# Kernel optimization log

Hardware: AMD Instinct MI355X
Metric: run time of the kernel (lower is better)

Reference implementation:

```python
import jax, jax.numpy as jnp
import numpy as np
import math

D_MODEL = 2048
NUM_HEADS = 32
NUM_KV_HEADS = 8
HEAD_DIM = D_MODEL // NUM_HEADS  # 64
BATCH = 2
SEQ = 2048


def setup_inputs() -> dict:
    key = jax.random.key(0)
    ks = jax.random.split(key, 5)
    std_q = math.sqrt(2.0 / (D_MODEL + D_MODEL))
    std_kv = math.sqrt(2.0 / (D_MODEL + NUM_KV_HEADS * HEAD_DIM))
    x = jax.random.normal(ks[0], (BATCH, SEQ, D_MODEL), dtype=jnp.float32)
    Wq = jax.random.normal(ks[1], (D_MODEL, D_MODEL), dtype=jnp.float32) * std_q
    Wk = jax.random.normal(ks[2], (NUM_KV_HEADS * HEAD_DIM, D_MODEL), dtype=jnp.float32) * std_kv
    Wv = jax.random.normal(ks[3], (NUM_KV_HEADS * HEAD_DIM, D_MODEL), dtype=jnp.float32) * std_kv
    Wo = jax.random.normal(ks[4], (D_MODEL, D_MODEL), dtype=jnp.float32) * std_q
    return {"x": x, "Wq": Wq, "Wk": Wk, "Wv": Wv, "Wo": Wo}


def reference(x, Wq, Wk, Wv, Wo):
    B, L, _ = x.shape
    group = NUM_HEADS // NUM_KV_HEADS
    # projections: x @ W.T
    q = (x @ Wq.T).reshape(B, L, NUM_HEADS, HEAD_DIM).transpose(0, 2, 1, 3)      # [B,H,L,D]
    k = (x @ Wk.T).reshape(B, L, NUM_KV_HEADS, HEAD_DIM).transpose(0, 2, 1, 3)   # [B,Hkv,L,D]
    v = (x @ Wv.T).reshape(B, L, NUM_KV_HEADS, HEAD_DIM).transpose(0, 2, 1, 3)
    # expand KV heads (repeat_interleave along head dim)
    k = jnp.repeat(k, group, axis=1)  # [B,H,L,D]
    v = jnp.repeat(v, group, axis=1)
    scale = 1.0 / math.sqrt(HEAD_DIM)
    scores = jnp.einsum("bhld,bhsd->bhls", q, k) * scale  # [B,H,L,S]
    causal_mask = jnp.tril(jnp.ones((L, L), dtype=bool))
    scores = jnp.where(causal_mask[None, None], scores, -jnp.inf)
    weights = jax.nn.softmax(scores, axis=-1)
    out = jnp.einsum("bhls,bhsd->bhld", weights, v)  # [B,H,L,D]
    out = out.transpose(0, 2, 1, 3).reshape(B, L, D_MODEL)
    return out @ Wo.T
```

## Files before the change

### kernel.cpp

```cpp
#include <hip/hip_runtime.h>
#include <stdint.h>


typedef unsigned short u16;
typedef short bf16x8 __attribute__((ext_vector_type(8)));
typedef float f32x4 __attribute__((ext_vector_type(4)));

#define D_MODEL 2048
#define QKV_DIM 3072
#define NUM_HEADS 32
#define HEAD_DIM 64
#define SEQ 2048
#define MTOT 4096

static __device__ __forceinline__ u16 f2bf(float f){
  uint32_t u = __builtin_bit_cast(uint32_t, f);
  u += 0x7FFFu + ((u >> 16) & 1u);
  return (u16)(u >> 16);
}

static __device__ __forceinline__ float exp2_fast(float x){
  float r;
  asm("v_exp_f32 %0, %1" : "=v"(r) : "v"(x));
  return r;
}

static __device__ __forceinline__ uint32_t cvt_pk_bf16(float lo, float hi){
  uint32_t r;
  asm("v_cvt_pk_bf16_f32 %0, %1, %2" : "=v"(r) : "v"(lo), "v"(hi));
  return r;
}

static __device__ __forceinline__ void gload16(const u16* g, u16* l){
  __builtin_amdgcn_global_load_lds(
      (__attribute__((address_space(1))) uint32_t*)(uintptr_t)g,
      (__attribute__((address_space(3))) uint32_t*)l,
      16, 0, 0);
}

__global__ __launch_bounds__(256)
void cvt_bf16(const float* __restrict__ in, u16* __restrict__ out, int n,
              float scl){
  const int i = (blockIdx.x * 256 + threadIdx.x) * 8;
  if (i >= n) return;
  float4 a = *(const float4*)(in + i);
  float4 b = *(const float4*)(in + i + 4);
  union { u16 h[8]; uint4 v; } t;
  t.h[0]=f2bf(a.x*scl); t.h[1]=f2bf(a.y*scl); t.h[2]=f2bf(a.z*scl); t.h[3]=f2bf(a.w*scl);
  t.h[4]=f2bf(b.x*scl); t.h[5]=f2bf(b.y*scl); t.h[6]=f2bf(b.z*scl); t.h[7]=f2bf(b.w*scl);
  *(uint4*)(out + i) = t.v;
}

template <bool F32OUT>
__global__ __launch_bounds__(256)
void gemm_bt(const u16* __restrict__ A, const u16* __restrict__ B,
             void* __restrict__ Cv, int M, int N, int K){
  constexpr int BK = 32;
  __shared__ __attribute__((aligned(16))) u16 As[128*BK];
  __shared__ __attribute__((aligned(16))) u16 Bs[128*BK];
  const int tid  = threadIdx.x;
  const int wave = tid >> 6, lane = tid & 63;
  const int quad = lane >> 4, l16 = lane & 15;
  const int wrow = wave >> 1, wcol = wave & 1;
  const int m0 = blockIdx.y * 128, n0 = blockIdx.x * 128;
  const int srow = lane >> 2, scol = (lane & 3) * 8;

  const f32x4 zero = {0.f, 0.f, 0.f, 0.f};
  f32x4 acc[4][4];
#pragma unroll
  for (int i = 0; i < 4; i++)
#pragma unroll
    for (int j = 0; j < 4; j++) acc[i][j] = zero;

  for (int k0 = 0; k0 < K; k0 += BK){
#pragma unroll
    for (int t = 0; t < 2; t++){
      const int chunk = wave + t*4;
      gload16(A + (size_t)(m0 + chunk*16 + srow)*K + k0 + scol, As + chunk*16*BK);
      gload16(B + (size_t)(n0 + chunk*16 + srow)*K + k0 + scol, Bs + chunk*16*BK);
    }
    __syncthreads();
    bf16x8 af[4], bfr[4];
#pragma unroll
    for (int mi = 0; mi < 4; mi++)
      af[mi] = *(const bf16x8*)(As + (wrow*64 + mi*16 + l16)*BK + quad*8);
#pragma unroll
    for (int ni = 0; ni < 4; ni++)
      bfr[ni] = *(const bf16x8*)(Bs + (wcol*64 + ni*16 + l16)*BK + quad*8);
#pragma unroll
    for (int mi = 0; mi < 4; mi++)
#pragma unroll
      for (int ni = 0; ni < 4; ni++)
        acc[mi][ni] = __builtin_amdgcn_mfma_f32_16x16x32_bf16(af[mi], bfr[ni], acc[mi][ni], 0, 0, 0);
    __syncthreads();
  }
#pragma unroll
  for (int mi = 0; mi < 4; mi++)
#pragma unroll
    for (int ni = 0; ni < 4; ni++){
      const int col = n0 + wcol*64 + ni*16 + l16;
#pragma unroll
      for (int r = 0; r < 4; r++){
        const int row = m0 + wrow*64 + mi*16 + quad*4 + r;
        if constexpr (F32OUT)
          ((float*)Cv)[(size_t)row*N + col] = acc[mi][ni][r];
        else
          ((u16*)Cv)[(size_t)row*N + col] = f2bf(acc[mi][ni][r]);
      }
    }
}

__global__ __launch_bounds__(256)
void kvtrans(const u16* __restrict__ QKV, u16* __restrict__ Ksw,
             u16* __restrict__ Vsw){
  __shared__ u16 Ls[64*72];
  const int tid = threadIdx.x;
  const int st = blockIdx.x, hk = blockIdx.y, b = blockIdx.z;
  const size_t rb = (size_t)b * SEQ;
  const size_t tbase = ((size_t)(b*8 + hk)*32 + st) * 4096;

#pragma unroll
  for (int t = 0; t < 2; t++){
    const int task = t*256 + tid;
    const int r = task >> 3, c = task & 7;
    uint4 kv = *(const uint4*)(QKV + (rb + st*64 + r)*QKV_DIM + 2048 + hk*HEAD_DIM + c*8);
    *(uint4*)(Ksw + tbase + r*64 + (size_t)((c ^ (r & 7)) * 8)) = kv;
  }
#pragma unroll
  for (int t = 0; t < 2; t++){
    const int task = t*256 + tid;
    const int r = task >> 3, c = task & 7;
    *(uint4*)(Ls + r*72 + c*8) =
        *(const uint4*)(QKV + (rb + st*64 + r)*QKV_DIM + 2560 + hk*HEAD_DIM + c*8);
  }
  __syncthreads();
#pragma unroll
  for (int t = 0; t < 2; t++){
    const int task = t*256 + tid;
    const int d = task >> 3, sc = task & 7;
    union { u16 h[8]; uint4 v; } tmp;
#pragma unroll
    for (int e = 0; e < 8; e++){
      const int key = ((2*(sc>>2) + (e>>2))<<4) + ((sc&3)<<2) + (e&3);
      tmp.h[e] = Ls[key*72 + d];
    }
    *(uint4*)(Vsw + tbase + d*64 + (size_t)((sc ^ (d & 7)) * 8)) = tmp.v;
  }
}

__global__ __launch_bounds__(256)
void attn(const u16* __restrict__ Q, const u16* __restrict__ Ksw,
          const u16* __restrict__ Vsw, u16* __restrict__ O, int qs){
  __shared__ __attribute__((aligned(16))) u16 Ks[2][64*64];
  __shared__ __attribute__((aligned(16))) u16 Vt[2][64*64];
  const int tid = threadIdx.x;
  const int wave = tid >> 6, lane = tid & 63, quad = lane >> 4, l16 = lane & 15;
  const int g_ = (blockIdx.x + blockIdx.y) & 31;
  const int qt = blockIdx.z ? (31 - g_) : g_;
  const int h = blockIdx.y, b = blockIdx.z;
  const int hk = h >> 2;
  const size_t rb = (size_t)b * SEQ;
  const size_t hb = ((size_t)(b*8 + hk)) * 32;

  const int qrow = wave*16 + l16;
  const int sw = l16 & 7;

  bf16x8 qf[2];
  {
    const u16* qp = Q + (rb + qt*64 + wave*16 + l16)*qs + h*HEAD_DIM;
    qf[0] = *(const bf16x8*)(qp + quad*8);
    qf[1] = *(const bf16x8*)(qp + 32 + quad*8);
  }
  const f32x4 zero = {0.f, 0.f, 0.f, 0.f};
  f32x4 oacc[4];
#pragma unroll
  for (int i = 0; i < 4; i++) oacc[i] = zero;
  float m_i = -INFINITY;
  float l_i = 0.f;

  {
    const u16* kt = Ksw + hb * 4096;
    const u16* vt = Vsw + hb * 4096;
#pragma unroll
    for (int t = 0; t < 2; t++){
      const int ch = wave*2 + t;
      gload16(kt + ch*512 + lane*8, &Ks[0][ch*512]);
      gload16(vt + ch*512 + lane*8, &Vt[0][ch*512]);
    }
  }
  int cur = 0;

  for (int j = 0; j <= qt; ++j){
    __syncthreads();
    if (j < qt){
      const u16* kt = Ksw + (hb + j + 1) * 4096;
      const u16* vt = Vsw + (hb + j + 1) * 4096;
#pragma unroll
      for (int t = 0; t < 2; t++){
        const int ch = wave*2 + t;
        gload16(kt + ch*512 + lane*8, &Ks[cur^1][ch*512]);
        gload16(vt + ch*512 + lane*8, &Vt[cur^1][ch*512]);
      }
    }
    const u16* Ksb = Ks[cur];
    const u16* Vtb = Vt[cur];

    f32x4 st[4];
#pragma unroll
    for (int ni = 0; ni < 4; ni++){
      f32x4 s = zero;
#pragma unroll
      for (int ss = 0; ss < 2; ss++){
        bf16x8 kf = *(const bf16x8*)(Ksb + ((ni*16 + l16) << 6) +
                                     (((ss*4 + quad) ^ sw) << 3));
        s = __builtin_amdgcn_mfma_f32_16x16x32_bf16(kf, qf[ss], s, 0, 0, 0);
      }
      st[ni] = s;
    }
    if (j == qt){
#pragma unroll
      for (int ni = 0; ni < 4; ni++)
#pragma unroll
        for (int r = 0; r < 4; r++)
          if (ni*16 + quad*4 + r > qrow) st[ni][r] = -INFINITY;
    }

    float mx = fmaxf(fmaxf(fmaxf(st[0][0], st[0][1]), fmaxf(st[0][2], st[0][3])),
                     fmaxf(fmaxf(st[1][0], st[1][1]), fmaxf(st[1][2], st[1][3])));
    mx = fmaxf(mx, fmaxf(fmaxf(fmaxf(st[2][0], st[2][1]), fmaxf(st[2][2], st[2][3])),
                         fmaxf(fmaxf(st[3][0], st[3][1]), fmaxf(st[3][2], st[3][3]))));
    mx = fmaxf(mx, __shfl_xor(mx, 16));
    mx = fmaxf(mx, __shfl_xor(mx, 32));

    if (__all(mx <= m_i + 10.f)){
      float ps = 0.f;
#pragma unroll
      for (int ni = 0; ni < 4; ni++)
#pragma unroll
        for (int r = 0; r < 4; r++){
          const float p = exp2_fast(st[ni][r] - m_i);
          st[ni][r] = p;
          ps += p;
        }
      ps += __shfl_xor(ps, 16);
      ps += __shfl_xor(ps, 32);
      l_i += ps;
    } else {
      const float mn = fmaxf(m_i, mx);
      const float alpha = exp2_fast(m_i - mn);
      float ps = 0.f;
#pragma unroll
      for (int ni = 0; ni < 4; ni++)
#pragma unroll
        for (int r = 0; r < 4; r++){
          const float p = exp2_fast(st[ni][r] - mn);
          st[ni][r] = p;
          ps += p;
        }
      ps += __shfl_xor(ps, 16);
      ps += __shfl_xor(ps, 32);
      l_i = l_i*alpha + ps;
      m_i = mn;
      float ar[4];
#pragma unroll
      for (int r = 0; r < 4; r++) ar[r] = __shfl(alpha, quad*4 + r);
#pragma unroll
      for (int ci = 0; ci < 4; ci++)
#pragma unroll
        for (int r = 0; r < 4; r++) oacc[ci][r] *= ar[r];
    }

    bf16x8 pfr[2];
#pragma unroll
    for (int ss = 0; ss < 2; ss++){
      union { uint32_t w[4]; bf16x8 v; } pk;
      pk.w[0] = cvt_pk_bf16(st[2*ss][0],   st[2*ss][1]);
      pk.w[1] = cvt_pk_bf16(st[2*ss][2],   st[2*ss][3]);
      pk.w[2] = cvt_pk_bf16(st[2*ss+1][0], st[2*ss+1][1]);
      pk.w[3] = cvt_pk_bf16(st[2*ss+1][2], st[2*ss+1][3]);
      pfr[ss] = pk.v;
    }

#pragma unroll
    for (int ss = 0; ss < 2; ss++)
#pragma unroll
      for (int ci = 0; ci < 4; ci++){
        bf16x8 vf = *(const bf16x8*)(Vtb + ((ci*16 + l16) << 6) +
                                     (((ss*4 + quad) ^ sw) << 3));
        oacc[ci] = __builtin_amdgcn_mfma_f32_16x16x32_bf16(pfr[ss], vf, oacc[ci], 0, 0, 0);
      }
    cur ^= 1;
  }

  float lf[4];
#pragma unroll
  for (int r = 0; r < 4; r++) lf[r] = __shfl(l_i, quad*4 + r);
#pragma unroll
  for (int ci = 0; ci < 4; ci++)
#pragma unroll
    for (int r = 0; r < 4; r++){
      const size_t row = rb + qt*64 + wave*16 + quad*4 + r;
      O[row*D_MODEL + h*HEAD_DIM + ci*16 + l16] = f2bf(oacc[ci][r] / lf[r]);
    }
}

extern "C" void kernel_launch(void* const* d_in, const int* in_sizes, int n_in,
                              void* d_out, int out_size, void* d_ws, size_t ws_size,
                              hipStream_t stream){
  const float* x  = (const float*)d_in[0];
  const float* Wq = (const float*)d_in[1];
  const float* Wk = (const float*)d_in[2];
  const float* Wv = (const float*)d_in[3];
  const float* Wo = (const float*)d_in[4];
  float* out = (float*)d_out;

  u16* xb   = (u16*)d_ws;
  u16* Wb   = xb + (size_t)MTOT*D_MODEL;
  u16* QKVb = (u16*)d_out;
  u16* Kswz = Wb;
  u16* Vswz = Wb + (size_t)2*1024*1024;

  const int nx  = MTOT*D_MODEL;
  const int nwq = D_MODEL*D_MODEL;
  const int nwk = 512*D_MODEL;
  const float QSCL = 0.125f * 1.44269504f;

  cvt_bf16<<<nx/2048, 256, 0, stream>>>(x, xb, nx, 1.0f);
  cvt_bf16<<<nwq/2048, 256, 0, stream>>>(Wq, Wb, nwq, QSCL);
  cvt_bf16<<<nwk/2048, 256, 0, stream>>>(Wk, Wb + (size_t)D_MODEL*D_MODEL, nwk, 1.0f);
  cvt_bf16<<<nwk/2048, 256, 0, stream>>>(Wv, Wb + (size_t)2560*D_MODEL, nwk, 1.0f);
  gemm_bt<false><<<dim3(QKV_DIM/128, MTOT/128), 256, 0, stream>>>(xb, Wb, QKVb, MTOT, QKV_DIM, D_MODEL);
  kvtrans<<<dim3(SEQ/64, 8, 2), 256, 0, stream>>>(QKVb, Kswz, Vswz);
  attn<<<dim3(SEQ/64, NUM_HEADS, 2), 256, 0, stream>>>(
      QKVb, Kswz, Vswz, xb, QKV_DIM);
  cvt_bf16<<<nwq/2048, 256, 0, stream>>>(Wo, Wb, nwq, 1.0f);
  gemm_bt<true><<<dim3(D_MODEL/128, MTOT/128), 256, 0, stream>>>(xb, Wb, (void*)out, MTOT, D_MODEL, D_MODEL);
}
```

Baseline: 341.4 us.

## Process two query heads per attention block and double GEMM K-tile depth

The attention kernel now handles two query heads that share one KV head in each block. Each K/V tile loaded into shared memory is reused for both heads, which halves the grid and the KV traffic per head. Separately, the GEMM K-tile grows from 32 to 64, with the load indexing reworked, so there are fewer sync barriers per K. The costs are more registers per thread, a doubled LDS footprint in the GEMM, and possible bank conflicts from the unswizzled wider rows.

```diff
diff --git a/kernel.cpp b/kernel.cpp
--- a/kernel.cpp
+++ b/kernel.cpp
@@ -55,7 +55,7 @@
 __global__ __launch_bounds__(256)
 void gemm_bt(const u16* __restrict__ A, const u16* __restrict__ B,
              void* __restrict__ Cv, int M, int N, int K){
-  constexpr int BK = 32;
+  constexpr int BK = 64;
   __shared__ __attribute__((aligned(16))) u16 As[128*BK];
   __shared__ __attribute__((aligned(16))) u16 Bs[128*BK];
   const int tid  = threadIdx.x;
@@ -63,7 +63,7 @@
   const int quad = lane >> 4, l16 = lane & 15;
   const int wrow = wave >> 1, wcol = wave & 1;
   const int m0 = blockIdx.y * 128, n0 = blockIdx.x * 128;
-  const int srow = lane >> 2, scol = (lane & 3) * 8;
+  const int srow = lane >> 3, scol = (lane & 7) * 8;
 
   const f32x4 zero = {0.f, 0.f, 0.f, 0.f};
   f32x4 acc[4][4];
@@ -74,24 +74,30 @@
 
   for (int k0 = 0; k0 < K; k0 += BK){
 #pragma unroll
-    for (int t = 0; t < 2; t++){
-      const int chunk = wave + t*4;
-      gload16(A + (size_t)(m0 + chunk*16 + srow)*K + k0 + scol, As + chunk*16*BK);
-      gload16(B + (size_t)(n0 + chunk*16 + srow)*K + k0 + scol, Bs + chunk*16*BK);
+    for (int t = 0; t < 4; t++){
+      const int c = wave*4 + t;
+      gload16(A + (size_t)(m0 + c*8 + srow)*K + k0 + scol, As + c*512);
+      gload16(B + (size_t)(n0 + c*8 + srow)*K + k0 + scol, Bs + c*512);
     }
     __syncthreads();
-    bf16x8 af[4], bfr[4];
+    bf16x8 af[4][2], bfr[4][2];
 #pragma unroll
     for (int mi = 0; mi < 4; mi++)
-      af[mi] = *(const bf16x8*)(As + (wrow*64 + mi*16 + l16)*BK + quad*8);
+#pragma unroll
+      for (int kk = 0; kk < 2; kk++)
+        af[mi][kk] = *(const bf16x8*)(As + (wrow*64 + mi*16 + l16)*BK + kk*32 + quad*8);
 #pragma unroll
     for (int ni = 0; ni < 4; ni++)
-      bfr[ni] = *(const bf16x8*)(Bs + (wcol*64 + ni*16 + l16)*BK + quad*8);
+#pragma unroll
+      for (int kk = 0; kk < 2; kk++)
+        bfr[ni][kk] = *(const bf16x8*)(Bs + (wcol*64 + ni*16 + l16)*BK + kk*32 + quad*8);
 #pragma unroll
     for (int mi = 0; mi < 4; mi++)
 #pragma unroll
       for (int ni = 0; ni < 4; ni++)
-        acc[mi][ni] = __builtin_amdgcn_mfma_f32_16x16x32_bf16(af[mi], bfr[ni], acc[mi][ni], 0, 0, 0);
+#pragma unroll
+        for (int kk = 0; kk < 2; kk++)
+          acc[mi][ni] = __builtin_amdgcn_mfma_f32_16x16x32_bf16(af[mi][kk], bfr[ni][kk], acc[mi][ni], 0, 0, 0);
     __syncthreads();
   }
 #pragma unroll
@@ -146,6 +152,95 @@
     }
     *(uint4*)(Vsw + tbase + d*64 + (size_t)((sc ^ (d & 7)) * 8)) = tmp.v;
   }
+}
+
+static __device__ __forceinline__ void head_step(
+    const u16* __restrict__ Ksb, const u16* __restrict__ Vtb,
+    const bf16x8* qf, f32x4* oacc, float& m_i, float& l_i,
+    int quad, int l16, int sw, bool diag, int qrow){
+  const f32x4 zero = {0.f, 0.f, 0.f, 0.f};
+  f32x4 st[4];
+#pragma unroll
+  for (int ni = 0; ni < 4; ni++){
+    f32x4 s = zero;
+#pragma unroll
+    for (int ss = 0; ss < 2; ss++){
+      bf16x8 kf = *(const bf16x8*)(Ksb + ((ni*16 + l16) << 6) +
+                                   (((ss*4 + quad) ^ sw) << 3));
+      s = __builtin_amdgcn_mfma_f32_16x16x32_bf16(kf, qf[ss], s, 0, 0, 0);
+    }
+    st[ni] = s;
+  }
+  if (diag){
+#pragma unroll
+    for (int ni = 0; ni < 4; ni++)
+#pragma unroll
+      for (int r = 0; r < 4; r++)
+        if (ni*16 + quad*4 + r > qrow) st[ni][r] = -INFINITY;
+  }
+  float mx = fmaxf(fmaxf(fmaxf(st[0][0], st[0][1]), fmaxf(st[0][2], st[0][3])),
+                   fmaxf(fmaxf(st[1][0], st[1][1]), fmaxf(st[1][2], st[1][3])));
+  mx = fmaxf(mx, fmaxf(fmaxf(fmaxf(st[2][0], st[2][1]), fmaxf(st[2][2], st[2][3])),
+                       fmaxf(fmaxf(st[3][0], st[3][1]), fmaxf(st[3][2], st[3][3]))));
+  mx = fmaxf(mx, __shfl_xor(mx, 16));
+  mx = fmaxf(mx, __shfl_xor(mx, 32));
+
+  if (__all(mx <= m_i + 10.f)){
+    float ps = 0.f;
+#pragma unroll
+    for (int ni = 0; ni < 4; ni++)
+#pragma unroll
+      for (int r = 0; r < 4; r++){
+        const float p = exp2_fast(st[ni][r] - m_i);
+        st[ni][r] = p;
+        ps += p;
+      }
+    ps += __shfl_xor(ps, 16);
+    ps += __shfl_xor(ps, 32);
+    l_i += ps;
+  } else {
+    const float mn = fmaxf(m_i, mx);
+    const float alpha = exp2_fast(m_i - mn);
+    float ps = 0.f;
+#pragma unroll
+    for (int ni = 0; ni < 4; ni++)
+#pragma unroll
+      for (int r = 0; r < 4; r++){
+        const float p = exp2_fast(st[ni][r] - mn);
+        st[ni][r] = p;
+        ps += p;
+      }
+    ps += __shfl_xor(ps, 16);
+    ps += __shfl_xor(ps, 32);
+    l_i = l_i*alpha + ps;
+    m_i = mn;
+    float ar[4];
+#pragma unroll
+    for (int r = 0; r < 4; r++) ar[r] = __shfl(alpha, quad*4 + r);
+#pragma unroll
+    for (int ci = 0; ci < 4; ci++)
+#pragma unroll
+      for (int r = 0; r < 4; r++) oacc[ci][r] *= ar[r];
+  }
+
+  bf16x8 pfr[2];
+#pragma unroll
+  for (int ss = 0; ss < 2; ss++){
+    union { uint32_t w[4]; bf16x8 v; } pk;
+    pk.w[0] = cvt_pk_bf16(st[2*ss][0],   st[2*ss][1]);
+    pk.w[1] = cvt_pk_bf16(st[2*ss][2],   st[2*ss][3]);
+    pk.w[2] = cvt_pk_bf16(st[2*ss+1][0], st[2*ss+1][1]);
+    pk.w[3] = cvt_pk_bf16(st[2*ss+1][2], st[2*ss+1][3]);
+    pfr[ss] = pk.v;
+  }
+#pragma unroll
+  for (int ss = 0; ss < 2; ss++)
+#pragma unroll
+    for (int ci = 0; ci < 4; ci++){
+      bf16x8 vf = *(const bf16x8*)(Vtb + ((ci*16 + l16) << 6) +
+                                   (((ss*4 + quad) ^ sw) << 3));
+      oacc[ci] = __builtin_amdgcn_mfma_f32_16x16x32_bf16(pfr[ss], vf, oacc[ci], 0, 0, 0);
+    }
 }
 
 __global__ __launch_bounds__(256)
@@ -157,26 +252,29 @@
   const int wave = tid >> 6, lane = tid & 63, quad = lane >> 4, l16 = lane & 15;
   const int g_ = (blockIdx.x + blockIdx.y) & 31;
   const int qt = blockIdx.z ? (31 - g_) : g_;
-  const int h = blockIdx.y, b = blockIdx.z;
-  const int hk = h >> 2;
+  const int hp = blockIdx.y, b = blockIdx.z;
+  const int h0 = hp*2, h1 = h0 + 1;
+  const int hk = hp >> 1;
   const size_t rb = (size_t)b * SEQ;
   const size_t hb = ((size_t)(b*8 + hk)) * 32;
 
   const int qrow = wave*16 + l16;
   const int sw = l16 & 7;
 
-  bf16x8 qf[2];
+  bf16x8 qfA[2], qfB[2];
   {
-    const u16* qp = Q + (rb + qt*64 + wave*16 + l16)*qs + h*HEAD_DIM;
-    qf[0] = *(const bf16x8*)(qp + quad*8);
-    qf[1] = *(const bf16x8*)(qp + 32 + quad*8);
+    const u16* qpA = Q + (rb + qt*64 + wave*16 + l16)*qs + h0*HEAD_DIM;
+    qfA[0] = *(const bf16x8*)(qpA + quad*8);
+    qfA[1] = *(const bf16x8*)(qpA + 32 + quad*8);
+    const u16* qpB = Q + (rb + qt*64 + wave*16 + l16)*qs + h1*HEAD_DIM;
+    qfB[0] = *(const bf16x8*)(qpB + quad*8);
+    qfB[1] = *(const bf16x8*)(qpB + 32 + quad*8);
   }
   const f32x4 zero = {0.f, 0.f, 0.f, 0.f};
-  f32x4 oacc[4];
-#pragma unroll
-  for (int i = 0; i < 4; i++) oacc[i] = zero;
-  float m_i = -INFINITY;
-  float l_i = 0.f;
+  f32x4 oA[4], oB[4];
+#pragma unroll
+  for (int i = 0; i < 4; i++){ oA[i] = zero; oB[i] = zero; }
+  float mA = -INFINITY, lA = 0.f, mB = -INFINITY, lB = 0.f;
 
   {
     const u16* kt = Ksw + hb * 4096;
@@ -204,103 +302,26 @@
     }
     const u16* Ksb = Ks[cur];
     const u16* Vtb = Vt[cur];
-
-    f32x4 st[4];
-#pragma unroll
-    for (int ni = 0; ni < 4; ni++){
-      f32x4 s = zero;
-#pragma unroll
-      for (int ss = 0; ss < 2; ss++){
-        bf16x8 kf = *(const bf16x8*)(Ksb + ((ni*16 + l16) << 6) +
-                                     (((ss*4 + quad) ^ sw) << 3));
-        s = __builtin_amdgcn_mfma_f32_16x16x32_bf16(kf, qf[ss], s, 0, 0, 0);
-      }
-      st[ni] = s;
-    }
-    if (j == qt){
-#pragma unroll
-      for (int ni = 0; ni < 4; ni++)
-#pragma unroll
-        for (int r = 0; r < 4; r++)
-          if (ni*16 + quad*4 + r > qrow) st[ni][r] = -INFINITY;
-    }
-
-    float mx = fmaxf(fmaxf(fmaxf(st[0][0], st[0][1]), fmaxf(st[0][2], st[0][3])),
-                     fmaxf(fmaxf(st[1][0], st[1][1]), fmaxf(st[1][2], st[1][3])));
-    mx = fmaxf(mx, fmaxf(fmaxf(fmaxf(st[2][0], st[2][1]), fmaxf(st[2][2], st[2][3])),
-                         fmaxf(fmaxf(st[3][0], st[3][1]), fmaxf(st[3][2], st[3][3]))));
-    mx = fmaxf(mx, __shfl_xor(mx, 16));
-    mx = fmaxf(mx, __shfl_xor(mx, 32));
-
-    if (__all(mx <= m_i + 10.f)){
-      float ps = 0.f;
-#pragma unroll
-      for (int ni = 0; ni < 4; ni++)
-#pragma unroll
-        for (int r = 0; r < 4; r++){
-          const float p = exp2_fast(st[ni][r] - m_i);
-          st[ni][r] = p;
-          ps += p;
-        }
-      ps += __shfl_xor(ps, 16);
-      ps += __shfl_xor(ps, 32);
-      l_i += ps;
-    } else {
-      const float mn = fmaxf(m_i, mx);
-      const float alpha = exp2_fast(m_i - mn);
-      float ps = 0.f;
-#pragma unroll
-      for (int ni = 0; ni < 4; ni++)
-#pragma unroll
-        for (int r = 0; r < 4; r++){
-          const float p = exp2_fast(st[ni][r] - mn);
-          st[ni][r] = p;
-          ps += p;
-        }
-      ps += __shfl_xor(ps, 16);
-      ps += __shfl_xor(ps, 32);
-      l_i = l_i*alpha + ps;
-      m_i = mn;
-      float ar[4];
-#pragma unroll
-      for (int r = 0; r < 4; r++) ar[r] = __shfl(alpha, quad*4 + r);
-#pragma unroll
-      for (int ci = 0; ci < 4; ci++)
-#pragma unroll
-        for (int r = 0; r < 4; r++) oacc[ci][r] *= ar[r];
-    }
-
-    bf16x8 pfr[2];
-#pragma unroll
-    for (int ss = 0; ss < 2; ss++){
-      union { uint32_t w[4]; bf16x8 v; } pk;
-      pk.w[0] = cvt_pk_bf16(st[2*ss][0],   st[2*ss][1]);
-      pk.w[1] = cvt_pk_bf16(st[2*ss][2],   st[2*ss][3]);
-      pk.w[2] = cvt_pk_bf16(st[2*ss+1][0], st[2*ss+1][1]);
-      pk.w[3] = cvt_pk_bf16(st[2*ss+1][2], st[2*ss+1][3]);
-      pfr[ss] = pk.v;
-    }
-
-#pragma unroll
-    for (int ss = 0; ss < 2; ss++)
-#pragma unroll
-      for (int ci = 0; ci < 4; ci++){
-        bf16x8 vf = *(const bf16x8*)(Vtb + ((ci*16 + l16) << 6) +
-                                     (((ss*4 + quad) ^ sw) << 3));
-        oacc[ci] = __builtin_amdgcn_mfma_f32_16x16x32_bf16(pfr[ss], vf, oacc[ci], 0, 0, 0);
-      }
+    const bool diag = (j == qt);
+
+    head_step(Ksb, Vtb, qfA, oA, mA, lA, quad, l16, sw, diag, qrow);
+    head_step(Ksb, Vtb, qfB, oB, mB, lB, quad, l16, sw, diag, qrow);
     cur ^= 1;
   }
 
-  float lf[4];
-#pragma unroll
-  for (int r = 0; r < 4; r++) lf[r] = __shfl(l_i, quad*4 + r);
+  float lfA[4], lfB[4];
+#pragma unroll
+  for (int r = 0; r < 4; r++){
+    lfA[r] = __shfl(lA, quad*4 + r);
+    lfB[r] = __shfl(lB, quad*4 + r);
+  }
 #pragma unroll
   for (int ci = 0; ci < 4; ci++)
 #pragma unroll
     for (int r = 0; r < 4; r++){
       const size_t row = rb + qt*64 + wave*16 + quad*4 + r;
-      O[row*D_MODEL + h*HEAD_DIM + ci*16 + l16] = f2bf(oacc[ci][r] / lf[r]);
+      O[row*D_MODEL + h0*HEAD_DIM + ci*16 + l16] = f2bf(oA[ci][r] / lfA[r]);
+      O[row*D_MODEL + h1*HEAD_DIM + ci*16 + l16] = f2bf(oB[ci][r] / lfB[r]);
     }
 }
 
@@ -331,7 +352,7 @@
   cvt_bf16<<<nwk/2048, 256, 0, stream>>>(Wv, Wb + (size_t)2560*D_MODEL, nwk, 1.0f);
   gemm_bt<false><<<dim3(QKV_DIM/128, MTOT/128), 256, 0, stream>>>(xb, Wb, QKVb, MTOT, QKV_DIM, D_MODEL);
   kvtrans<<<dim3(SEQ/64, 8, 2), 256, 0, stream>>>(QKVb, Kswz, Vswz);
-  attn<<<dim3(SEQ/64, NUM_HEADS, 2), 256, 0, stream>>>(
+  attn<<<dim3(SEQ/64, NUM_HEADS/2, 2), 256, 0, stream>>>(
       QKVb, Kswz, Vswz, xb, QKV_DIM);
   cvt_bf16<<<nwq/2048, 256, 0, stream>>>(Wo, Wb, nwq, 1.0f);
   gemm_bt<true><<<dim3(D_MODEL/128, MTOT/128), 256, 0, stream>>>(xb, Wb, (void*)out, MTOT, D_MODEL, D_MODEL);
```

Measured after the change: 382.5 us. +12.1%, slower.

## Fuse all fp32-to-bf16 conversions into one launch and remap GEMM tiles per XCD

Applied to the files above, without the earlier changes.

The separate conversion kernels for x, Wq, Wk, Wv and, when workspace allows, Wo are merged into a single launch. This removes several launch gaps and the standalone Wo conversion between attention and the output projection. Both GEMMs now use a 1D grid whose block IDs are remapped so consecutive tiles land on the same XCD, aiming for better L2 reuse of the A and B panels. The cost is some branching per block and a workspace-size dependent fallback path.

```diff
diff --git a/kernel.cpp b/kernel.cpp
--- a/kernel.cpp
+++ b/kernel.cpp
@@ -38,23 +38,46 @@
       16, 0, 0);
 }
 
+static __device__ __forceinline__ void cvt8(const float* __restrict__ src,
+                                            u16* __restrict__ dst,
+                                            int i, float scl){
+  float4 a = *(const float4*)(src + i);
+  float4 b = *(const float4*)(src + i + 4);
+  union { u16 h[8]; uint4 v; } t;
+  t.h[0]=f2bf(a.x*scl); t.h[1]=f2bf(a.y*scl); t.h[2]=f2bf(a.z*scl); t.h[3]=f2bf(a.w*scl);
+  t.h[4]=f2bf(b.x*scl); t.h[5]=f2bf(b.y*scl); t.h[6]=f2bf(b.z*scl); t.h[7]=f2bf(b.w*scl);
+  *(uint4*)(dst + i) = t.v;
+}
+
 __global__ __launch_bounds__(256)
 void cvt_bf16(const float* __restrict__ in, u16* __restrict__ out, int n,
               float scl){
   const int i = (blockIdx.x * 256 + threadIdx.x) * 8;
   if (i >= n) return;
-  float4 a = *(const float4*)(in + i);
-  float4 b = *(const float4*)(in + i + 4);
-  union { u16 h[8]; uint4 v; } t;
-  t.h[0]=f2bf(a.x*scl); t.h[1]=f2bf(a.y*scl); t.h[2]=f2bf(a.z*scl); t.h[3]=f2bf(a.w*scl);
-  t.h[4]=f2bf(b.x*scl); t.h[5]=f2bf(b.y*scl); t.h[6]=f2bf(b.z*scl); t.h[7]=f2bf(b.w*scl);
-  *(uint4*)(out + i) = t.v;
+  cvt8(in, out, i, scl);
+}
+
+__global__ __launch_bounds__(256)
+void cvt_all(const float* __restrict__ x,  const float* __restrict__ Wq,
+             const float* __restrict__ Wk, const float* __restrict__ Wv,
+             const float* __restrict__ Wo,
+             u16* __restrict__ xb, u16* __restrict__ Wb,
+             u16* __restrict__ Wob, float qscl){
+  const int bid = blockIdx.x;
+  const float* src; u16* dst; int off; float scl = 1.0f;
+  if (bid < 4096){        src = x;  dst = xb;                              off = bid;        }
+  else if (bid < 6144){   src = Wq; dst = Wb;                              off = bid - 4096; scl = qscl; }
+  else if (bid < 6656){   src = Wk; dst = Wb + (size_t)D_MODEL*D_MODEL;    off = bid - 6144; }
+  else if (bid < 7168){   src = Wv; dst = Wb + (size_t)2560*D_MODEL;       off = bid - 6656; }
+  else {                  src = Wo; dst = Wob;                             off = bid - 7168; }
+  const int i = (off * 256 + threadIdx.x) * 8;
+  cvt8(src, dst, i, scl);
 }
 
 template <bool F32OUT>
 __global__ __launch_bounds__(256)
 void gemm_bt(const u16* __restrict__ A, const u16* __restrict__ B,
-             void* __restrict__ Cv, int M, int N, int K){
+             void* __restrict__ Cv, int M, int N, int K, int nbx){
   constexpr int BK = 32;
   __shared__ __attribute__((aligned(16))) u16 As[128*BK];
   __shared__ __attribute__((aligned(16))) u16 Bs[128*BK];
@@ -62,7 +85,11 @@
   const int wave = tid >> 6, lane = tid & 63;
   const int quad = lane >> 4, l16 = lane & 15;
   const int wrow = wave >> 1, wcol = wave & 1;
-  const int m0 = blockIdx.y * 128, n0 = blockIdx.x * 128;
+  const int nwg = gridDim.x;
+  const int qq = nwg >> 3, rr = nwg & 7;
+  const int xcd = blockIdx.x & 7, lin = blockIdx.x >> 3;
+  const int swz = (xcd < rr ? xcd*(qq+1) : rr*(qq+1) + (xcd-rr)*qq) + lin;
+  const int m0 = (swz / nbx) * 128, n0 = (swz % nbx) * 128;
   const int srow = lane >> 2, scol = (lane & 3) * 8;
 
   const f32x4 zero = {0.f, 0.f, 0.f, 0.f};
@@ -316,23 +343,35 @@
 
   u16* xb   = (u16*)d_ws;
   u16* Wb   = xb + (size_t)MTOT*D_MODEL;
+  u16* Wob  = Wb + (size_t)QKV_DIM*D_MODEL;
   u16* QKVb = (u16*)d_out;
   u16* Kswz = Wb;
   u16* Vswz = Wb + (size_t)2*1024*1024;
 
-  const int nx  = MTOT*D_MODEL;
   const int nwq = D_MODEL*D_MODEL;
-  const int nwk = 512*D_MODEL;
   const float QSCL = 0.125f * 1.44269504f;
 
-  cvt_bf16<<<nx/2048, 256, 0, stream>>>(x, xb, nx, 1.0f);
-  cvt_bf16<<<nwq/2048, 256, 0, stream>>>(Wq, Wb, nwq, QSCL);
-  cvt_bf16<<<nwk/2048, 256, 0, stream>>>(Wk, Wb + (size_t)D_MODEL*D_MODEL, nwk, 1.0f);
-  cvt_bf16<<<nwk/2048, 256, 0, stream>>>(Wv, Wb + (size_t)2560*D_MODEL, nwk, 1.0f);
-  gemm_bt<false><<<dim3(QKV_DIM/128, MTOT/128), 256, 0, stream>>>(xb, Wb, QKVb, MTOT, QKV_DIM, D_MODEL);
+  const size_t ws_need = ((size_t)MTOT*D_MODEL + (size_t)QKV_DIM*D_MODEL +
+                          (size_t)D_MODEL*D_MODEL) * sizeof(u16);
+  const bool wob_fits = (ws_size >= ws_need);
+
+  if (wob_fits){
+    cvt_all<<<9216, 256, 0, stream>>>(x, Wq, Wk, Wv, Wo, xb, Wb, Wob, QSCL);
+  } else {
+    cvt_all<<<7168, 256, 0, stream>>>(x, Wq, Wk, Wv, Wo, xb, Wb, Wob, QSCL);
+  }
+  gemm_bt<false><<<(QKV_DIM/128)*(MTOT/128), 256, 0, stream>>>(
+      xb, Wb, QKVb, MTOT, QKV_DIM, D_MODEL, QKV_DIM/128);
   kvtrans<<<dim3(SEQ/64, 8, 2), 256, 0, stream>>>(QKVb, Kswz, Vswz);
   attn<<<dim3(SEQ/64, NUM_HEADS, 2), 256, 0, stream>>>(
       QKVb, Kswz, Vswz, xb, QKV_DIM);
-  cvt_bf16<<<nwq/2048, 256, 0, stream>>>(Wo, Wb, nwq, 1.0f);
-  gemm_bt<true><<<dim3(D_MODEL/128, MTOT/128), 256, 0, stream>>>(xb, Wb, (void*)out, MTOT, D_MODEL, D_MODEL);
-}
+  const u16* Bw2;
+  if (wob_fits){
+    Bw2 = Wob;
+  } else {
+    cvt_bf16<<<nwq/2048, 256, 0, stream>>>(Wo, Wb, nwq, 1.0f);
+    Bw2 = Wb;
+  }
+  gemm_bt<true><<<(D_MODEL/128)*(MTOT/128), 256, 0, stream>>>(
+      xb, Bw2, (void*)out, MTOT, D_MODEL, D_MODEL, D_MODEL/128);
+}
```

Result: faster. 326.3 us (-4.4%).
